# Optimization experiments

Hardware: AMD Instinct MI355X
Metric: run time of the kernel (lower is better)

The kernel has to match this reference:

```python
import jax, jax.numpy as jnp
import numpy as np

B = 65536      # batch of (state, action) pairs
DIM_S = 64     # input feature dim
DIM_C = 8      # number of options / experts
H = 256        # hidden width (two hidden layers)


def setup_inputs() -> dict:
    key = jax.random.key(0)
    ks = jax.random.split(key, 7)
    s = 0.05  # small init scale
    st = jax.random.normal(ks[0], (B, DIM_S), dtype=jnp.float32)
    # Batched expert weights: one slice per expert (dim_c experts).
    W1 = jax.random.normal(ks[1], (DIM_C, DIM_S, H), dtype=jnp.float32) * s
    b1 = jax.random.normal(ks[2], (DIM_C, H), dtype=jnp.float32) * s
    W2 = jax.random.normal(ks[3], (DIM_C, H, H), dtype=jnp.float32) * s
    b2 = jax.random.normal(ks[4], (DIM_C, H), dtype=jnp.float32) * s
    W3 = jax.random.normal(ks[5], (DIM_C, H, 1), dtype=jnp.float32) * s
    b3 = jax.random.normal(ks[6], (DIM_C, 1), dtype=jnp.float32) * s
    return {"st": st, "W1": W1, "b1": b1, "W2": W2, "b2": b2,
            "W3": W3, "b3": b3}


def reference(st, W1, b1, W2, b2, W3, b3):
    # Equivalent of torch.stack([m(st) for m in self.discriminator], dim=1):
    # every expert MLP (dim_s -> H -> H -> 1, ReLU) applied to the same st,
    # expressed as batched GEMMs over the expert axis c.
    h = jax.nn.relu(jnp.einsum('bs,csh->bch', st, W1) + b1[None])   # [B, C, H]
    h = jax.nn.relu(jnp.einsum('bch,chk->bck', h, W2) + b2[None])   # [B, C, H]
    d = jnp.einsum('bch,cho->bco', h, W3) + b3[None]                # [B, C, 1]
    return d
```

## Files before the change

### kernel.cpp

```cpp
#include <hip/hip_runtime.h>
#include <hip/hip_bf16.h>

typedef __bf16 bf16x8 __attribute__((ext_vector_type(8)));
typedef float  f32x4  __attribute__((ext_vector_type(4)));
typedef float  f32x16 __attribute__((ext_vector_type(16)));

static constexpr int S  = 64;
static constexpr int C  = 8;
static constexpr int HD = 256;

__device__ __forceinline__ unsigned short f2bf(float f) {
  __hip_bfloat16 b = __float2bfloat16(f);
  unsigned short u;
  __builtin_memcpy(&u, &b, 2);
  return u;
}

__device__ __forceinline__ void gl2lds16(const void* g, void* l) {
  __builtin_amdgcn_global_load_lds(
      (const __attribute__((address_space(1))) unsigned int*)g,
      (__attribute__((address_space(3))) unsigned int*)l, 16, 0, 0);
}

__global__ __launch_bounds__(256) void prep_frags(
    const float* __restrict__ W1, const float* __restrict__ W2,
    unsigned short* __restrict__ W1F, unsigned short* __restrict__ W2F)
{
  const int g = blockIdx.x * 256 + threadIdx.x;
  if (blockIdx.x < 256) {
    const int c  = g >> 13, rem = g & 8191;
    const int fg = rem >> 6, l = rem & 63;
    const int ct = fg >> 4, stp = fg & 15;
    const int k0 = stp * 16 + (l >> 5) * 8;
    const int n  = ct * 32 + (l & 31);
    const float* src = W2 + ((size_t)c * 256 + k0) * 256 + n;
    unsigned short* dst = W2F + (size_t)c * 65536 + (size_t)(fg * 64 + l) * 8;
    #pragma unroll
    for (int e = 0; e < 8; ++e) dst[e] = f2bf(src[(size_t)e * 256]);
  } else {
    const int gg = g - 65536;
    const int c  = gg >> 11, rem = gg & 2047;
    const int fg = rem >> 6, l = rem & 63;
    const int mt = fg >> 2, ks = fg & 3;
    const int s0 = ks * 16 + (l >> 5) * 8;
    const int h  = mt * 32 + (l & 31);
    const float* src = W1 + ((size_t)c * 64 + s0) * 256 + h;
    unsigned short* dst = W1F + (size_t)c * 16384 + (size_t)(fg * 64 + l) * 8;
    #pragma unroll
    for (int e = 0; e < 8; ++e) dst[e] = f2bf(src[(size_t)e * 256]);
  }
}

__global__ __launch_bounds__(512, 2) void moe_fused(
    const float* __restrict__ st,
    const unsigned short* __restrict__ W1F,
    const unsigned short* __restrict__ W2F,
    const float* __restrict__ b1,
    const float* __restrict__ b2,
    const float* __restrict__ W3,
    const float* __restrict__ b3,
    float* __restrict__ out)
{
  __shared__ __align__(16) unsigned short sW2[HD * HD];

  const int tid  = threadIdx.x;
  const int lane = tid & 63;
  const int wv   = tid >> 6;
  const int l31  = lane & 31;
  const int h5   = lane >> 5;

  const int b    = blockIdx.x;
  const int x    = b & 7;
  const int m    = b >> 3;
  const int c    = m & 7;
  const int sgrp = m >> 3;

  const unsigned short* W1c = W1F + (size_t)c * 16384;
  const unsigned short* W2c = W2F + (size_t)c * 65536;

  #pragma unroll
  for (int it = 0; it < 16; ++it) {
    const int slot = it * 8 + wv;
    gl2lds16(W2c + slot * 512 + lane * 8, sW2 + slot * 512);
  }

  float b2v[8], w3v[8];
  #pragma unroll
  for (int ct = 0; ct < 8; ++ct) {
    b2v[ct] = b2[c * HD + ct * 32 + l31];
    w3v[ct] = W3[c * HD + ct * 32 + l31];
  }
  const float bb3 = b3[c];

  bool need_bar = true;

  for (int ji = 0; ji < 4; ++ji) {
    const int tile = x * 16 + sgrp * 4 + ji;
    const int wrow = tile * 512 + wv * 64;

    bf16x8 bB[4][2];
    #pragma unroll
    for (int nt = 0; nt < 2; ++nt) {
      #pragma unroll
      for (int ks = 0; ks < 4; ++ks) {
        const float* rp = st + (size_t)(wrow + nt * 32 + l31) * S + ks * 16 + h5 * 8;
        float4 xx = *reinterpret_cast<const float4*>(rp);
        float4 yy = *reinterpret_cast<const float4*>(rp + 4);
        union { bf16x8 v; unsigned short us[8]; } pk;
        pk.us[0] = f2bf(xx.x); pk.us[1] = f2bf(xx.y); pk.us[2] = f2bf(xx.z); pk.us[3] = f2bf(xx.w);
        pk.us[4] = f2bf(yy.x); pk.us[5] = f2bf(yy.y); pk.us[6] = f2bf(yy.z); pk.us[7] = f2bf(yy.w);
        bB[ks][nt] = pk.v;
      }
    }

    bf16x8 aF[2][16];
    #pragma unroll
    for (int mt = 0; mt < 8; ++mt) {
      f32x16 acc0 = {}, acc1 = {};
      #pragma unroll
      for (int ks = 0; ks < 4; ++ks) {
        bf16x8 aW = *reinterpret_cast<const bf16x8*>(
            W1c + (size_t)((mt * 4 + ks) * 64 + lane) * 8);
        acc0 = __builtin_amdgcn_mfma_f32_32x32x16_bf16(aW, bB[ks][0], acc0, 0, 0, 0);
        acc1 = __builtin_amdgcn_mfma_f32_32x32x16_bf16(aW, bB[ks][1], acc1, 0, 0, 0);
      }
      f32x4 bias[4];
      #pragma unroll
      for (int gq = 0; gq < 4; ++gq)
        bias[gq] = *reinterpret_cast<const f32x4*>(
            b1 + c * HD + mt * 32 + 8 * gq + 4 * h5);

      #pragma unroll
      for (int rt = 0; rt < 2; ++rt) {
        const f32x16& A = rt ? acc1 : acc0;
        unsigned d[8];
        #pragma unroll
        for (int p = 0; p < 8; ++p) {
          float v0 = A[2 * p]     + bias[p >> 1][2 * (p & 1)];
          float v1 = A[2 * p + 1] + bias[p >> 1][2 * (p & 1) + 1];
          v0 = v0 > 0.f ? v0 : 0.f;
          v1 = v1 > 0.f ? v1 : 0.f;
          __asm__("v_cvt_pk_bf16_f32 %0, %1, %2" : "=v"(d[p]) : "v"(v0), "v"(v1));
        }
        __asm__("v_permlane32_swap_b32 %0, %1" : "+v"(d[0]), "+v"(d[2]));
        __asm__("v_permlane32_swap_b32 %0, %1" : "+v"(d[1]), "+v"(d[3]));
        __asm__("v_permlane32_swap_b32 %0, %1" : "+v"(d[4]), "+v"(d[6]));
        __asm__("v_permlane32_swap_b32 %0, %1" : "+v"(d[5]), "+v"(d[7]));
        union { unsigned u[4]; bf16x8 v; } f0, f1;
        f0.u[0] = d[0]; f0.u[1] = d[1]; f0.u[2] = d[2]; f0.u[3] = d[3];
        f1.u[0] = d[4]; f1.u[1] = d[5]; f1.u[2] = d[6]; f1.u[3] = d[7];
        aF[rt][2 * mt]     = f0.v;
        aF[rt][2 * mt + 1] = f1.v;
      }
    }

    if (need_bar) {
      __syncthreads();
      need_bar = false;
    }

    float dacc0[16], dacc1[16];
    #pragma unroll
    for (int r = 0; r < 16; ++r) { dacc0[r] = 0.f; dacc1[r] = 0.f; }

    #pragma unroll
    for (int ct = 0; ct < 8; ++ct) {
      f32x16 acc0 = {}, acc1 = {};
      #pragma unroll
      for (int s2 = 0; s2 < 16; ++s2) {
        bf16x8 bF = *reinterpret_cast<const bf16x8*>(
            sW2 + (size_t)((ct * 16 + s2) * 64 + lane) * 8);
        acc0 = __builtin_amdgcn_mfma_f32_32x32x16_bf16(aF[0][s2], bF, acc0, 0, 0, 0);
        acc1 = __builtin_amdgcn_mfma_f32_32x32x16_bf16(aF[1][s2], bF, acc1, 0, 0, 0);
      }
      #pragma unroll
      for (int r = 0; r < 16; ++r) {
        float v0 = acc0[r] + b2v[ct]; v0 = v0 > 0.f ? v0 : 0.f; dacc0[r] += v0 * w3v[ct];
        float v1 = acc1[r] + b2v[ct]; v1 = v1 > 0.f ? v1 : 0.f; dacc1[r] += v1 * w3v[ct];
      }
    }

    #pragma unroll
    for (int r = 0; r < 16; ++r) {
      float v0 = dacc0[r], v1 = dacc1[r];
      v0 += __shfl_xor(v0, 1);  v1 += __shfl_xor(v1, 1);
      v0 += __shfl_xor(v0, 2);  v1 += __shfl_xor(v1, 2);
      v0 += __shfl_xor(v0, 4);  v1 += __shfl_xor(v1, 4);
      v0 += __shfl_xor(v0, 8);  v1 += __shfl_xor(v1, 8);
      v0 += __shfl_xor(v0, 16); v1 += __shfl_xor(v1, 16);
      dacc0[r] = v0; dacc1[r] = v1;
    }

    if (l31 == 0) {
      #pragma unroll
      for (int r = 0; r < 16; ++r) {
        const int rr = (r & 3) + 8 * (r >> 2) + 4 * h5;
        out[(size_t)(wrow + rr) * C + c]      = dacc0[r] + bb3;
        out[(size_t)(wrow + 32 + rr) * C + c] = dacc1[r] + bb3;
      }
    }
  }
}

extern "C" void kernel_launch(void* const* d_in, const int* in_sizes, int n_in,
                              void* d_out, int out_size, void* d_ws, size_t ws_size,
                              hipStream_t stream)
{
  const float* st = (const float*)d_in[0];
  const float* W1 = (const float*)d_in[1];
  const float* b1 = (const float*)d_in[2];
  const float* W2 = (const float*)d_in[3];
  const float* b2 = (const float*)d_in[4];
  const float* W3 = (const float*)d_in[5];
  const float* b3 = (const float*)d_in[6];
  float* out = (float*)d_out;

  unsigned short* W1F = (unsigned short*)d_ws;
  unsigned short* W2F = W1F + C * HD * S;

  prep_frags<<<dim3(320), dim3(256), 0, stream>>>(W1, W2, W1F, W2F);
  moe_fused<<<dim3(256), dim3(512), 0, stream>>>(st, W1F, W2F, b1, b2, W3, b3, out);
}
```

Before: 194.6 us.

## Software-pipeline input, W1 and LDS W2 fragment loads and fold biases into MFMA init

Prefetches the next tile's st rows into registers during the current tile's compute, and double-buffers the W1 fragments from global memory and the W2 fragments from LDS so loads overlap MFMA work. Biases b1 and b2 are folded into the MFMA accumulator initial value, which removes the separate bias adds. MFMA runs are wrapped in s_setprio, and the input conversion uses packed bf16 converts. The extra prefetch registers raise VGPR pressure at 2 waves per SIMD and could cause spills.

```diff
diff --git a/kernel.cpp b/kernel.cpp
--- a/kernel.cpp
+++ b/kernel.cpp
@@ -78,6 +78,19 @@
   const unsigned short* W1c = W1F + (size_t)c * 16384;
   const unsigned short* W2c = W2F + (size_t)c * 65536;
 
+  float4 sraw[16];
+  {
+    const int wr0 = (x * 16 + sgrp * 4) * 512 + wv * 64;
+    #pragma unroll
+    for (int nt = 0; nt < 2; ++nt)
+      #pragma unroll
+      for (int ks = 0; ks < 4; ++ks) {
+        const float* rp = st + (size_t)(wr0 + nt * 32 + l31) * S + ks * 16 + h5 * 8;
+        sraw[(nt * 4 + ks) * 2]     = *reinterpret_cast<const float4*>(rp);
+        sraw[(nt * 4 + ks) * 2 + 1] = *reinterpret_cast<const float4*>(rp + 4);
+      }
+  }
+
   #pragma unroll
   for (int it = 0; it < 16; ++it) {
     const int slot = it * 8 + wv;
@@ -92,43 +105,54 @@
   }
   const float bb3 = b3[c];
 
-  bool need_bar = true;
-
   for (int ji = 0; ji < 4; ++ji) {
     const int tile = x * 16 + sgrp * 4 + ji;
     const int wrow = tile * 512 + wv * 64;
 
     bf16x8 bB[4][2];
     #pragma unroll
-    for (int nt = 0; nt < 2; ++nt) {
+    for (int nt = 0; nt < 2; ++nt)
       #pragma unroll
       for (int ks = 0; ks < 4; ++ks) {
-        const float* rp = st + (size_t)(wrow + nt * 32 + l31) * S + ks * 16 + h5 * 8;
-        float4 xx = *reinterpret_cast<const float4*>(rp);
-        float4 yy = *reinterpret_cast<const float4*>(rp + 4);
-        union { bf16x8 v; unsigned short us[8]; } pk;
-        pk.us[0] = f2bf(xx.x); pk.us[1] = f2bf(xx.y); pk.us[2] = f2bf(xx.z); pk.us[3] = f2bf(xx.w);
-        pk.us[4] = f2bf(yy.x); pk.us[5] = f2bf(yy.y); pk.us[6] = f2bf(yy.z); pk.us[7] = f2bf(yy.w);
+        float4 xx = sraw[(nt * 4 + ks) * 2];
+        float4 yy = sraw[(nt * 4 + ks) * 2 + 1];
+        union { bf16x8 v; unsigned u[4]; } pk;
+        __asm__("v_cvt_pk_bf16_f32 %0, %1, %2" : "=v"(pk.u[0]) : "v"(xx.x), "v"(xx.y));
+        __asm__("v_cvt_pk_bf16_f32 %0, %1, %2" : "=v"(pk.u[1]) : "v"(xx.z), "v"(xx.w));
+        __asm__("v_cvt_pk_bf16_f32 %0, %1, %2" : "=v"(pk.u[2]) : "v"(yy.x), "v"(yy.y));
+        __asm__("v_cvt_pk_bf16_f32 %0, %1, %2" : "=v"(pk.u[3]) : "v"(yy.z), "v"(yy.w));
         bB[ks][nt] = pk.v;
       }
-    }
 
     bf16x8 aF[2][16];
+    bf16x8 aWc[4], aWn[4];
+    #pragma unroll
+    for (int ks = 0; ks < 4; ++ks)
+      aWc[ks] = *reinterpret_cast<const bf16x8*>(W1c + (size_t)(ks * 64 + lane) * 8);
+
     #pragma unroll
     for (int mt = 0; mt < 8; ++mt) {
-      f32x16 acc0 = {}, acc1 = {};
-      #pragma unroll
-      for (int ks = 0; ks < 4; ++ks) {
-        bf16x8 aW = *reinterpret_cast<const bf16x8*>(
-            W1c + (size_t)((mt * 4 + ks) * 64 + lane) * 8);
-        acc0 = __builtin_amdgcn_mfma_f32_32x32x16_bf16(aW, bB[ks][0], acc0, 0, 0, 0);
-        acc1 = __builtin_amdgcn_mfma_f32_32x32x16_bf16(aW, bB[ks][1], acc1, 0, 0, 0);
-      }
-      f32x4 bias[4];
+      if (mt < 7) {
+        #pragma unroll
+        for (int ks = 0; ks < 4; ++ks)
+          aWn[ks] = *reinterpret_cast<const bf16x8*>(
+              W1c + (size_t)(((mt + 1) * 4 + ks) * 64 + lane) * 8);
+      }
+      union { f32x4 q[4]; f32x16 v; } bu;
       #pragma unroll
       for (int gq = 0; gq < 4; ++gq)
-        bias[gq] = *reinterpret_cast<const f32x4*>(
+        bu.q[gq] = *reinterpret_cast<const f32x4*>(
             b1 + c * HD + mt * 32 + 8 * gq + 4 * h5);
+
+      __builtin_amdgcn_s_setprio(1);
+      f32x16 acc0 = __builtin_amdgcn_mfma_f32_32x32x16_bf16(aWc[0], bB[0][0], bu.v, 0, 0, 0);
+      f32x16 acc1 = __builtin_amdgcn_mfma_f32_32x32x16_bf16(aWc[0], bB[0][1], bu.v, 0, 0, 0);
+      #pragma unroll
+      for (int ks = 1; ks < 4; ++ks) {
+        acc0 = __builtin_amdgcn_mfma_f32_32x32x16_bf16(aWc[ks], bB[ks][0], acc0, 0, 0, 0);
+        acc1 = __builtin_amdgcn_mfma_f32_32x32x16_bf16(aWc[ks], bB[ks][1], acc1, 0, 0, 0);
+      }
+      __builtin_amdgcn_s_setprio(0);
 
       #pragma unroll
       for (int rt = 0; rt < 2; ++rt) {
@@ -136,10 +160,8 @@
         unsigned d[8];
         #pragma unroll
         for (int p = 0; p < 8; ++p) {
-          float v0 = A[2 * p]     + bias[p >> 1][2 * (p & 1)];
-          float v1 = A[2 * p + 1] + bias[p >> 1][2 * (p & 1) + 1];
-          v0 = v0 > 0.f ? v0 : 0.f;
-          v1 = v1 > 0.f ? v1 : 0.f;
+          float v0 = A[2 * p];     v0 = v0 > 0.f ? v0 : 0.f;
+          float v1 = A[2 * p + 1]; v1 = v1 > 0.f ? v1 : 0.f;
           __asm__("v_cvt_pk_bf16_f32 %0, %1, %2" : "=v"(d[p]) : "v"(v0), "v"(v1));
         }
         __asm__("v_permlane32_swap_b32 %0, %1" : "+v"(d[0]), "+v"(d[2]));
@@ -152,12 +174,18 @@
         aF[rt][2 * mt]     = f0.v;
         aF[rt][2 * mt + 1] = f1.v;
       }
-    }
-
-    if (need_bar) {
-      __syncthreads();
-      need_bar = false;
-    }
+      if (mt < 7) {
+        #pragma unroll
+        for (int ks = 0; ks < 4; ++ks) aWc[ks] = aWn[ks];
+      }
+    }
+
+    if (ji == 0) __syncthreads();
+
+    bf16x8 fA[8], fB[8];
+    #pragma unroll
+    for (int s = 0; s < 8; ++s)
+      fA[s] = *reinterpret_cast<const bf16x8*>(sW2 + (size_t)(s * 64 + lane) * 8);
 
     float dacc0[16], dacc1[16];
     #pragma unroll
@@ -165,19 +193,57 @@
 
     #pragma unroll
     for (int ct = 0; ct < 8; ++ct) {
-      f32x16 acc0 = {}, acc1 = {};
-      #pragma unroll
-      for (int s2 = 0; s2 < 16; ++s2) {
-        bf16x8 bF = *reinterpret_cast<const bf16x8*>(
-            sW2 + (size_t)((ct * 16 + s2) * 64 + lane) * 8);
-        acc0 = __builtin_amdgcn_mfma_f32_32x32x16_bf16(aF[0][s2], bF, acc0, 0, 0, 0);
-        acc1 = __builtin_amdgcn_mfma_f32_32x32x16_bf16(aF[1][s2], bF, acc1, 0, 0, 0);
-      }
+      #pragma unroll
+      for (int s = 0; s < 8; ++s)
+        fB[s] = *reinterpret_cast<const bf16x8*>(
+            sW2 + (size_t)((ct * 16 + 8 + s) * 64 + lane) * 8);
+
+      f32x16 b2i;
+      #pragma unroll
+      for (int r = 0; r < 16; ++r) b2i[r] = b2v[ct];
+
+      __builtin_amdgcn_s_setprio(1);
+      f32x16 acc0 = __builtin_amdgcn_mfma_f32_32x32x16_bf16(aF[0][0], fA[0], b2i, 0, 0, 0);
+      f32x16 acc1 = __builtin_amdgcn_mfma_f32_32x32x16_bf16(aF[1][0], fA[0], b2i, 0, 0, 0);
+      #pragma unroll
+      for (int s = 1; s < 8; ++s) {
+        acc0 = __builtin_amdgcn_mfma_f32_32x32x16_bf16(aF[0][s], fA[s], acc0, 0, 0, 0);
+        acc1 = __builtin_amdgcn_mfma_f32_32x32x16_bf16(aF[1][s], fA[s], acc1, 0, 0, 0);
+      }
+      __builtin_amdgcn_s_setprio(0);
+
+      if (ct < 7) {
+        #pragma unroll
+        for (int s = 0; s < 8; ++s)
+          fA[s] = *reinterpret_cast<const bf16x8*>(
+              sW2 + (size_t)(((ct + 1) * 16 + s) * 64 + lane) * 8);
+      }
+
+      __builtin_amdgcn_s_setprio(1);
+      #pragma unroll
+      for (int s = 0; s < 8; ++s) {
+        acc0 = __builtin_amdgcn_mfma_f32_32x32x16_bf16(aF[0][8 + s], fB[s], acc0, 0, 0, 0);
+        acc1 = __builtin_amdgcn_mfma_f32_32x32x16_bf16(aF[1][8 + s], fB[s], acc1, 0, 0, 0);
+      }
+      __builtin_amdgcn_s_setprio(0);
+
       #pragma unroll
       for (int r = 0; r < 16; ++r) {
-        float v0 = acc0[r] + b2v[ct]; v0 = v0 > 0.f ? v0 : 0.f; dacc0[r] += v0 * w3v[ct];
-        float v1 = acc1[r] + b2v[ct]; v1 = v1 > 0.f ? v1 : 0.f; dacc1[r] += v1 * w3v[ct];
-      }
+        float v0 = acc0[r]; v0 = v0 > 0.f ? v0 : 0.f; dacc0[r] += v0 * w3v[ct];
+        float v1 = acc1[r]; v1 = v1 > 0.f ? v1 : 0.f; dacc1[r] += v1 * w3v[ct];
+      }
+    }
+
+    if (ji < 3) {
+      const int wrn = (tile + 1) * 512 + wv * 64;
+      #pragma unroll
+      for (int nt = 0; nt < 2; ++nt)
+        #pragma unroll
+        for (int ks = 0; ks < 4; ++ks) {
+          const float* rp = st + (size_t)(wrn + nt * 32 + l31) * S + ks * 16 + h5 * 8;
+          sraw[(nt * 4 + ks) * 2]     = *reinterpret_cast<const float4*>(rp);
+          sraw[(nt * 4 + ks) * 2 + 1] = *reinterpret_cast<const float4*>(rp + 4);
+        }
     }
 
     #pragma unroll
```

Result: slower. 672.2 us (+245.5%).
